# Kernel tuning notes

Hardware: AMD Instinct MI355X
Metric: run time of the kernel (lower is better)

## Reference

```python
import jax, jax.numpy as jnp
import numpy as np

N, E, G = 100000, 3200000, 256
IN_C, HID = 3, 32


def setup_inputs() -> dict:
    key = jax.random.key(0)
    ks = jax.random.split(key, 10)
    x = jax.random.normal(ks[0], (N, IN_C), dtype=jnp.float32)
    edge_index = jax.random.randint(ks[1], (2, E), 0, N, dtype=jnp.int64)
    edge_weight = jax.random.uniform(ks[2], (E,), dtype=jnp.float32)
    batch = jnp.sort(jax.random.randint(ks[3], (N,), 0, G, dtype=jnp.int64))
    # GCNConv params (PyG: out = norm-agg(x @ W) + b), glorot-ish init
    W0 = jax.random.normal(ks[4], (IN_C, HID), dtype=jnp.float32) / np.sqrt(IN_C)
    b0 = jnp.zeros((HID,), dtype=jnp.float32)
    W1 = jax.random.normal(ks[5], (HID, HID), dtype=jnp.float32) / np.sqrt(HID)
    b1 = jnp.zeros((HID,), dtype=jnp.float32)
    Wr = jax.random.normal(ks[6], (HID, 1), dtype=jnp.float32) / np.sqrt(HID)
    br = jnp.zeros((1,), dtype=jnp.float32)
    return {"x": x, "edge_index": edge_index, "edge_weight": edge_weight,
            "batch": batch, "W0": W0, "b0": b0, "W1": W1, "b1": b1,
            "Wr": Wr, "br": br}


def _gcn_conv(x, row, col, w_edge, W, b, n_nodes):
    # PyG GCNConv with add_self_loops + symmetric normalization
    h = x @ W                                   # [N, H]
    deg = jax.ops.segment_sum(w_edge, col, num_segments=n_nodes)
    dinv = jnp.where(deg > 0, jax.lax.rsqrt(deg), 0.0)
    norm = dinv[row] * w_edge * dinv[col]       # [E+N]
    msg = h[row] * norm[:, None]                # gather + scale
    agg = jax.ops.segment_sum(msg, col, num_segments=n_nodes)
    return agg + b


def reference(x, edge_index, edge_weight, batch, W0, b0, W1, b1, Wr, br):
    n = x.shape[0]
    loop = jnp.arange(n, dtype=edge_index.dtype)
    row = jnp.concatenate([edge_index[0], loop])   # source (j)
    col = jnp.concatenate([edge_index[1], loop])   # target (i)
    w = jnp.concatenate([edge_weight, jnp.ones((n,), dtype=edge_weight.dtype)])

    h = jax.nn.relu(_gcn_conv(x, row, col, w, W0, b0, n))
    h = jax.nn.relu(_gcn_conv(h, row, col, w, W1, b1, n))

    # global_mean_pool over graphs
    ones = jnp.ones((n,), dtype=h.dtype)
    cnt = jax.ops.segment_sum(ones, batch, num_segments=G)
    summed = jax.ops.segment_sum(h, batch, num_segments=G)
    hg = summed / jnp.maximum(cnt, 1.0)[:, None]   # [G, H]
    return (hg @ Wr + br).squeeze(-1)              # [G]
```

## Files before the change

### kernel.cpp

```cpp
#include <hip/hip_runtime.h>
#include <hip/hip_fp16.h>


#define TPB 256
#define NBMAX 512
#define BSH 8
#define BSZ 256
#define CAP 9216
#define ST 1024
#define SV 16
#define STILE (ST * SV)

typedef unsigned long long u64;
union H8 { float4 f4; __half2 h2[4]; };
union H4 { u64 u; __half2 h2[2]; };
union HU { __half h; unsigned short u; };

__global__ void k_init(unsigned* cursor, float* gsum, float* gcnt, int nb, int g) {
    int t = threadIdx.x;
    for (int j = t; j < nb; j += blockDim.x) cursor[j] = 0u;
    for (int j = t; j < g; j += blockDim.x) { gsum[j] = 0.0f; gcnt[j] = 0.0f; }
}

__global__ void __launch_bounds__(1024) k_scat(const int* __restrict__ row,
                       const int* __restrict__ col, const float* __restrict__ w,
                       unsigned* cursor, int2* __restrict__ tmp, int nb, int e) {
    __shared__ unsigned cl[NBMAX];
    __shared__ unsigned bl[NBMAX];
    int t = threadIdx.x;
    for (int j = t; j < nb; j += ST) cl[j] = 0u;
    __syncthreads();
    const int4* c4 = (const int4*)col;
    int e4 = e >> 2;
    int base4 = blockIdx.x * (STILE >> 2);
    int4 cv[SV / 4];
    unsigned rk[SV];
    bool vld[SV / 4];
    #pragma unroll
    for (int v = 0; v < SV / 4; ++v) {
        int i4 = base4 + t + v * ST;
        vld[v] = (i4 < e4);
        if (vld[v]) {
            cv[v] = c4[i4];
            rk[4 * v + 0] = atomicAdd(&cl[cv[v].x >> BSH], 1u);
            rk[4 * v + 1] = atomicAdd(&cl[cv[v].y >> BSH], 1u);
            rk[4 * v + 2] = atomicAdd(&cl[cv[v].z >> BSH], 1u);
            rk[4 * v + 3] = atomicAdd(&cl[cv[v].w >> BSH], 1u);
        }
    }
    int tailc = -1; unsigned tailrk = 0; int taili = 0;
    if (blockIdx.x == 0) {
        int i = (e4 << 2) + t;
        if (i < e) { taili = i; tailc = col[i]; tailrk = atomicAdd(&cl[tailc >> BSH], 1u); }
    }
    __syncthreads();
    for (int j = t; j < nb; j += ST) {
        unsigned c = cl[j];
        bl[j] = c ? atomicAdd(&cursor[j], c) : 0u;
    }
    __syncthreads();
    const int4* r4 = (const int4*)row;
    const float4* w4 = (const float4*)w;
    #pragma unroll
    for (int v = 0; v < SV / 4; ++v) {
        if (vld[v]) {
            int i4 = base4 + t + v * ST;
            int4 rr = r4[i4];
            float4 ww = w4[i4];
            int c, b; unsigned lo;
            c = cv[v].x; b = c >> BSH; lo = bl[b] + rk[4 * v + 0];
            if (lo < CAP) tmp[(size_t)b * CAP + lo] =
                make_int2((int)(((unsigned)(c & 255) << 24) | (unsigned)rr.x), __float_as_int(ww.x));
            c = cv[v].y; b = c >> BSH; lo = bl[b] + rk[4 * v + 1];
            if (lo < CAP) tmp[(size_t)b * CAP + lo] =
                make_int2((int)(((unsigned)(c & 255) << 24) | (unsigned)rr.y), __float_as_int(ww.y));
            c = cv[v].z; b = c >> BSH; lo = bl[b] + rk[4 * v + 2];
            if (lo < CAP) tmp[(size_t)b * CAP + lo] =
                make_int2((int)(((unsigned)(c & 255) << 24) | (unsigned)rr.z), __float_as_int(ww.z));
            c = cv[v].w; b = c >> BSH; lo = bl[b] + rk[4 * v + 3];
            if (lo < CAP) tmp[(size_t)b * CAP + lo] =
                make_int2((int)(((unsigned)(c & 255) << 24) | (unsigned)rr.w), __float_as_int(ww.w));
        }
    }
    if (tailc >= 0) {
        int b = tailc >> BSH; unsigned lo = bl[b] + tailrk;
        if (lo < CAP) tmp[(size_t)b * CAP + lo] =
            make_int2((int)(((unsigned)(tailc & 255) << 24) | (unsigned)row[taili]),
                      __float_as_int(w[taili]));
    }
}

__global__ void __launch_bounds__(1024) k_conv(const int2* __restrict__ tmp,
                       const unsigned* __restrict__ cursor, unsigned* __restrict__ nodeinfo,
                       float* __restrict__ dinv, unsigned* __restrict__ arr, int n) {
    __shared__ unsigned cnt[BSZ];
    __shared__ float dw[BSZ];
    __shared__ unsigned cur[BSZ];
    int t = threadIdx.x, b = blockIdx.x;
    if (t < BSZ) { cnt[t] = 0u; dw[t] = 1.0f; }
    __syncthreads();
    unsigned cb = cursor[b]; if (cb > CAP) cb = CAP;
    size_t base = (size_t)b * CAP;
    for (unsigned k = t; k < cb; k += 1024) {
        int2 p = tmp[base + k];
        unsigned c = (unsigned)p.x >> 24;
        atomicAdd(&cnt[c], 1u);
        atomicAdd(&dw[c], __int_as_float(p.y));
    }
    __syncthreads();
    unsigned v = 0;
    if (t < BSZ) { v = cnt[t]; cur[t] = v; }
    __syncthreads();
    for (int off = 1; off < BSZ; off <<= 1) {
        unsigned u = (t < BSZ && t >= off) ? cur[t - off] : 0u;
        __syncthreads();
        if (t < BSZ) cur[t] += u;
        __syncthreads();
    }
    if (t < BSZ) {
        unsigned excl = cur[t] - v;
        int node = (b << BSH) + t;
        if (node < n) {
            unsigned cc = v > 1023u ? 1023u : v;
            nodeinfo[node] = (cc << 22) | (unsigned)(base + excl);
            dinv[node] = rsqrtf(dw[t]);
        }
        cur[t] = excl;
    }
    __syncthreads();
    for (unsigned k = t; k < cb; k += 1024) {
        int2 p = tmp[base + k];
        unsigned c = (unsigned)p.x >> 24;
        unsigned slot = atomicAdd(&cur[c], 1u);
        HU wu; wu.h = __float2half(__int_as_float(p.y));
        arr[base + slot] = ((unsigned)(wu.u & 0x7FFFu) << 17) | ((unsigned)p.x & 0x1FFFFu);
    }
}

__global__ void k_xw0(const float* __restrict__ x, const float* __restrict__ W0,
                      const float* __restrict__ dinv, float4* __restrict__ hw4, int n) {
    int t = blockIdx.x * blockDim.x + threadIdx.x;
    if (t >= n * 4) return;
    int i = t >> 2, q = t & 3;
    float x0 = x[i * 3 + 0], x1 = x[i * 3 + 1], x2 = x[i * 3 + 2];
    float di = dinv[i];
    int cb = q * 8;
    H8 u;
    #pragma unroll
    for (int j = 0; j < 4; ++j) {
        int c = cb + 2 * j;
        float a = di * (x0 * W0[c]     + x1 * W0[32 + c]     + x2 * W0[64 + c]);
        float b = di * (x0 * W0[c + 1] + x1 * W0[32 + c + 1] + x2 * W0[64 + c + 1]);
        u.h2[j] = __float22half2_rn(make_float2(a, b));
    }
    hw4[t] = u.f4;
}

#define EDGE_ACC(V) { \
    unsigned rr = (V) & 0x1FFFFu; \
    HU wu; wu.u = (unsigned short)((V) >> 17); \
    float wv = __half2float(wu.h); \
    H4 g; g.u = hw8[(rr << 3) + q]; \
    float2 f0 = __half22float2(g.h2[0]); \
    float2 f1 = __half22float2(g.h2[1]); \
    a0.x = fmaf(wv, f0.x, a0.x); a0.y = fmaf(wv, f0.y, a0.y); \
    a1.x = fmaf(wv, f1.x, a1.x); a1.y = fmaf(wv, f1.y, a1.y); }

__global__ void __launch_bounds__(256) k_agg1(const u64* __restrict__ hw8,
                      const unsigned* __restrict__ arr, const unsigned* __restrict__ nodeinfo,
                      const float* __restrict__ dinv, const float* __restrict__ W1,
                      const float* __restrict__ b0, u64* __restrict__ out8, int n) {
    __shared__ float W1s[1024];
    __shared__ float hl[32][33];
    int tid = threadIdx.x;
    for (int j = tid; j < 1024; j += 256) W1s[j] = W1[j];
    int t = blockIdx.x * 256 + tid;
    int i = t >> 3, q = t & 7;
    if (i >= n) i = n - 1;
    int li = tid >> 3;
    unsigned info = nodeinfo[i];
    unsigned k = info & 0x3FFFFFu;
    unsigned hi = k + (info >> 22);
    int idx = (i << 3) + q;
    H4 s; s.u = hw8[idx];
    float2 a0 = __half22float2(s.h2[0]);
    float2 a1 = __half22float2(s.h2[1]);
    for (; k + 8 <= hi; k += 8) {
        unsigned v0 = __builtin_nontemporal_load(arr + k + 0);
        unsigned v1 = __builtin_nontemporal_load(arr + k + 1);
        unsigned v2 = __builtin_nontemporal_load(arr + k + 2);
        unsigned v3 = __builtin_nontemporal_load(arr + k + 3);
        unsigned v4 = __builtin_nontemporal_load(arr + k + 4);
        unsigned v5 = __builtin_nontemporal_load(arr + k + 5);
        unsigned v6 = __builtin_nontemporal_load(arr + k + 6);
        unsigned v7 = __builtin_nontemporal_load(arr + k + 7);
        EDGE_ACC(v0) EDGE_ACC(v1) EDGE_ACC(v2) EDGE_ACC(v3)
        EDGE_ACC(v4) EDGE_ACC(v5) EDGE_ACC(v6) EDGE_ACC(v7)
    }
    for (; k < hi; ++k) {
        unsigned v = __builtin_nontemporal_load(arr + k);
        EDGE_ACC(v)
    }
    float di = dinv[i];
    int cb = q << 2;
    hl[li][cb + 0] = fmaxf(di * a0.x + b0[cb + 0], 0.0f);
    hl[li][cb + 1] = fmaxf(di * a0.y + b0[cb + 1], 0.0f);
    hl[li][cb + 2] = fmaxf(di * a1.x + b0[cb + 2], 0.0f);
    hl[li][cb + 3] = fmaxf(di * a1.y + b0[cb + 3], 0.0f);
    __syncthreads();
    float o0 = 0.0f, o1 = 0.0f, o2 = 0.0f, o3 = 0.0f;
    #pragma unroll
    for (int kk = 0; kk < 32; ++kk) {
        float hv = hl[li][kk];
        const float* wr = &W1s[(kk << 5) + cb];
        o0 = fmaf(hv, wr[0], o0);
        o1 = fmaf(hv, wr[1], o1);
        o2 = fmaf(hv, wr[2], o2);
        o3 = fmaf(hv, wr[3], o3);
    }
    H4 oh;
    oh.h2[0] = __float22half2_rn(make_float2(di * o0, di * o1));
    oh.h2[1] = __float22half2_rn(make_float2(di * o2, di * o3));
    out8[idx] = oh.u;
}

__global__ void __launch_bounds__(256) k_agg2(const u64* __restrict__ hw8,
                      const unsigned* __restrict__ arr, const unsigned* __restrict__ nodeinfo,
                      const float* __restrict__ dinv, const float* __restrict__ b1,
                      const float* __restrict__ Wr, const int* __restrict__ batch,
                      float* gsum, float* gcnt, int n) {
    int t = blockIdx.x * 256 + threadIdx.x;
    int i = t >> 3, q = t & 7;
    bool active = (i < n);
    int ii = active ? i : (n - 1);
    unsigned info = active ? nodeinfo[ii] : 0u;
    unsigned k = info & 0x3FFFFFu;
    unsigned hi = k + (info >> 22);
    int idx = (ii << 3) + q;
    H4 s; s.u = hw8[idx];
    float2 a0 = __half22float2(s.h2[0]);
    float2 a1 = __half22float2(s.h2[1]);
    for (; k + 8 <= hi; k += 8) {
        unsigned v0 = __builtin_nontemporal_load(arr + k + 0);
        unsigned v1 = __builtin_nontemporal_load(arr + k + 1);
        unsigned v2 = __builtin_nontemporal_load(arr + k + 2);
        unsigned v3 = __builtin_nontemporal_load(arr + k + 3);
        unsigned v4 = __builtin_nontemporal_load(arr + k + 4);
        unsigned v5 = __builtin_nontemporal_load(arr + k + 5);
        unsigned v6 = __builtin_nontemporal_load(arr + k + 6);
        unsigned v7 = __builtin_nontemporal_load(arr + k + 7);
        EDGE_ACC(v0) EDGE_ACC(v1) EDGE_ACC(v2) EDGE_ACC(v3)
        EDGE_ACC(v4) EDGE_ACC(v5) EDGE_ACC(v6) EDGE_ACC(v7)
    }
    for (; k < hi; ++k) {
        unsigned v = __builtin_nontemporal_load(arr + k);
        EDGE_ACC(v)
    }
    float di = dinv[ii];
    int cb = q << 2;
    float sp = 0.0f;
    sp = fmaf(fmaxf(di * a0.x + b1[cb + 0], 0.0f), Wr[cb + 0], sp);
    sp = fmaf(fmaxf(di * a0.y + b1[cb + 1], 0.0f), Wr[cb + 1], sp);
    sp = fmaf(fmaxf(di * a1.x + b1[cb + 2], 0.0f), Wr[cb + 2], sp);
    sp = fmaf(fmaxf(di * a1.y + b1[cb + 3], 0.0f), Wr[cb + 3], sp);
    if (!active) sp = 0.0f;
    sp += __shfl_xor(sp, 1);
    sp += __shfl_xor(sp, 2);
    sp += __shfl_xor(sp, 4);
    int b = active ? batch[ii] : -1;
    int b0v = __shfl(b, 0, 64);
    bool uniform = (b0v >= 0) && (__ballot(b == b0v) == 0xFFFFFFFFFFFFFFFFULL);
    if (uniform) {
        float tot = sp;
        tot += __shfl_xor(tot, 8);
        tot += __shfl_xor(tot, 16);
        tot += __shfl_xor(tot, 32);
        if ((threadIdx.x & 63) == 0) {
            atomicAdd(&gsum[b0v], tot);
            atomicAdd(&gcnt[b0v], 8.0f);
        }
    } else if (active && q == 0) {
        atomicAdd(&gsum[b], sp);
        atomicAdd(&gcnt[b], 1.0f);
    }
}

__global__ void k_final(const float* gsum, const float* gcnt, const float* __restrict__ br,
                        float* out, int g) {
    int i = blockIdx.x * blockDim.x + threadIdx.x;
    if (i < g) out[i] = gsum[i] / fmaxf(gcnt[i], 1.0f) + br[0];
}

extern "C" void kernel_launch(void* const* d_in, const int* in_sizes, int n_in,
                              void* d_out, int out_size, void* d_ws, size_t ws_size,
                              hipStream_t stream) {
    const float* x     = (const float*)d_in[0];
    const int*   ei    = (const int*)d_in[1];
    const float* ew    = (const float*)d_in[2];
    const int*   batch = (const int*)d_in[3];
    const float* W0    = (const float*)d_in[4];
    const float* b0    = (const float*)d_in[5];
    const float* W1    = (const float*)d_in[6];
    const float* b1    = (const float*)d_in[7];
    const float* Wr    = (const float*)d_in[8];
    const float* br    = (const float*)d_in[9];
    float* out = (float*)d_out;

    int n = in_sizes[0] / 3;
    int e = in_sizes[2];
    int g = out_size;
    const int* row = ei;
    const int* col = ei + e;
    int nb = (n + BSZ - 1) >> BSH;

    char* ws = (char*)d_ws;
    size_t off = 0;
    auto alloc = [&](size_t bytes) -> void* {
        void* p = ws + off;
        off += (bytes + 255) & ~(size_t)255;
        return p;
    };
    unsigned* cursor   = (unsigned*)alloc((size_t)NBMAX * 4);
    unsigned* nodeinfo = (unsigned*)alloc((size_t)n * 4);
    float*    dinv     = (float*)   alloc((size_t)n * 4);
    float*    gsum     = (float*)   alloc((size_t)g * 4);
    float*    gcnt     = (float*)   alloc((size_t)g * 4);
    unsigned* arr      = (unsigned*)alloc((size_t)nb * CAP * 4);
    char*     region   = (char*)    alloc((size_t)nb * CAP * 8);
    int2*   tmp  = (int2*)region;
    __half* hWh1 = (__half*)region;
    __half* hWh2 = (__half*)(region + (size_t)n * 64);
    (void)ws_size;

    int stiles = (e + STILE - 1) / STILE;
    int nq4    = (n * 4 + TPB - 1) / TPB;
    int nq8    = (n * 8 + TPB - 1) / TPB;

    k_init  <<<1,      1024, 0, stream>>>(cursor, gsum, gcnt, nb, g);
    k_scat  <<<stiles, ST,   0, stream>>>(row, col, ew, cursor, tmp, nb, e);
    k_conv  <<<nb,     1024, 0, stream>>>(tmp, cursor, nodeinfo, dinv, arr, n);
    k_xw0   <<<nq4,    TPB,  0, stream>>>(x, W0, dinv, (float4*)hWh1, n);
    k_agg1  <<<nq8,    TPB,  0, stream>>>((const u64*)hWh1, arr, nodeinfo, dinv, W1, b0, (u64*)hWh2, n);
    k_agg2  <<<nq8,    TPB,  0, stream>>>((const u64*)hWh2, arr, nodeinfo, dinv, b1, Wr, batch, gsum, gcnt, n);
    k_final <<<1,      TPB,  0, stream>>>(gsum, gcnt, br, out, g);
}
```

Before: 284.6 us.

## Pack degree count and weight into one 64-bit LDS atomic, split pooling kernel

The scatter kernel's block size drops from 1024 to 512 threads. In the conversion kernel, the per-node edge count and weight sum are packed into one 64-bit shared-memory atomic, with the weight held as 24-bit fixed point, so each edge does one atomic instead of two. The global mean pooling moves out of the second aggregation kernel into a separate kernel that reads one scalar per node, so 64 nodes share a wave's atomics instead of 8. This costs an extra launch and a per-node buffer, and the fixed-point weight sum loses some precision.

```diff
diff --git a/kernel.cpp b/kernel.cpp
--- a/kernel.cpp
+++ b/kernel.cpp
@@ -7,7 +7,7 @@
 #define BSH 8
 #define BSZ 256
 #define CAP 9216
-#define ST 1024
+#define ST 512
 #define SV 16
 #define STILE (ST * SV)
 
@@ -22,7 +22,7 @@
     for (int j = t; j < g; j += blockDim.x) { gsum[j] = 0.0f; gcnt[j] = 0.0f; }
 }
 
-__global__ void __launch_bounds__(1024) k_scat(const int* __restrict__ row,
+__global__ void __launch_bounds__(ST) k_scat(const int* __restrict__ row,
                        const int* __restrict__ col, const float* __restrict__ w,
                        unsigned* cursor, int2* __restrict__ tmp, int nb, int e) {
     __shared__ unsigned cl[NBMAX];
@@ -93,23 +93,29 @@
 __global__ void __launch_bounds__(1024) k_conv(const int2* __restrict__ tmp,
                        const unsigned* __restrict__ cursor, unsigned* __restrict__ nodeinfo,
                        float* __restrict__ dinv, unsigned* __restrict__ arr, int n) {
-    __shared__ unsigned cnt[BSZ];
-    __shared__ float dw[BSZ];
+    __shared__ u64 pk[BSZ];
     __shared__ unsigned cur[BSZ];
     int t = threadIdx.x, b = blockIdx.x;
-    if (t < BSZ) { cnt[t] = 0u; dw[t] = 1.0f; }
+    if (t < BSZ) pk[t] = (u64)(1u << 24);
     __syncthreads();
     unsigned cb = cursor[b]; if (cb > CAP) cb = CAP;
     size_t base = (size_t)b * CAP;
     for (unsigned k = t; k < cb; k += 1024) {
         int2 p = tmp[base + k];
         unsigned c = (unsigned)p.x >> 24;
-        atomicAdd(&cnt[c], 1u);
-        atomicAdd(&dw[c], __int_as_float(p.y));
+        u64 add = (1ull << 48) |
+                  (u64)(unsigned)__float2uint_rn(__int_as_float(p.y) * 16777216.0f);
+        atomicAdd(&pk[c], add);
     }
     __syncthreads();
     unsigned v = 0;
-    if (t < BSZ) { v = cnt[t]; cur[t] = v; }
+    float dwv = 1.0f;
+    if (t < BSZ) {
+        u64 p = pk[t];
+        v = (unsigned)(p >> 48);
+        dwv = (float)(p & 0xFFFFFFFFFFFFull) * (1.0f / 16777216.0f);
+        cur[t] = v;
+    }
     __syncthreads();
     for (int off = 1; off < BSZ; off <<= 1) {
         unsigned u = (t < BSZ && t >= off) ? cur[t - off] : 0u;
@@ -123,7 +129,7 @@
         if (node < n) {
             unsigned cc = v > 1023u ? 1023u : v;
             nodeinfo[node] = (cc << 22) | (unsigned)(base + excl);
-            dinv[node] = rsqrtf(dw[t]);
+            dinv[node] = rsqrtf(dwv);
         }
         cur[t] = excl;
     }
@@ -227,13 +233,12 @@
 __global__ void __launch_bounds__(256) k_agg2(const u64* __restrict__ hw8,
                       const unsigned* __restrict__ arr, const unsigned* __restrict__ nodeinfo,
                       const float* __restrict__ dinv, const float* __restrict__ b1,
-                      const float* __restrict__ Wr, const int* __restrict__ batch,
-                      float* gsum, float* gcnt, int n) {
+                      const float* __restrict__ Wr, float* __restrict__ sout, int n) {
     int t = blockIdx.x * 256 + threadIdx.x;
     int i = t >> 3, q = t & 7;
     bool active = (i < n);
     int ii = active ? i : (n - 1);
-    unsigned info = active ? nodeinfo[ii] : 0u;
+    unsigned info = nodeinfo[ii];
     unsigned k = info & 0x3FFFFFu;
     unsigned hi = k + (info >> 22);
     int idx = (ii << 3) + q;
@@ -263,23 +268,28 @@
     sp = fmaf(fmaxf(di * a0.y + b1[cb + 1], 0.0f), Wr[cb + 1], sp);
     sp = fmaf(fmaxf(di * a1.x + b1[cb + 2], 0.0f), Wr[cb + 2], sp);
     sp = fmaf(fmaxf(di * a1.y + b1[cb + 3], 0.0f), Wr[cb + 3], sp);
-    if (!active) sp = 0.0f;
     sp += __shfl_xor(sp, 1);
     sp += __shfl_xor(sp, 2);
     sp += __shfl_xor(sp, 4);
-    int b = active ? batch[ii] : -1;
+    if (active && q == 0) sout[i] = sp;
+}
+
+__global__ void k_pool2(const float* __restrict__ sarr, const int* __restrict__ batch,
+                        float* gsum, float* gcnt, int n) {
+    int i = blockIdx.x * blockDim.x + threadIdx.x;
+    float sp = 0.0f;
+    int b = -1;
+    if (i < n) { sp = sarr[i]; b = batch[i]; }
     int b0v = __shfl(b, 0, 64);
     bool uniform = (b0v >= 0) && (__ballot(b == b0v) == 0xFFFFFFFFFFFFFFFFULL);
     if (uniform) {
-        float tot = sp;
-        tot += __shfl_xor(tot, 8);
-        tot += __shfl_xor(tot, 16);
-        tot += __shfl_xor(tot, 32);
+        #pragma unroll
+        for (int off = 32; off > 0; off >>= 1) sp += __shfl_down(sp, off, 64);
         if ((threadIdx.x & 63) == 0) {
-            atomicAdd(&gsum[b0v], tot);
-            atomicAdd(&gcnt[b0v], 8.0f);
+            atomicAdd(&gsum[b0v], sp);
+            atomicAdd(&gcnt[b0v], 64.0f);
         }
-    } else if (active && q == 0) {
+    } else if (i < n) {
         atomicAdd(&gsum[b], sp);
         atomicAdd(&gcnt[b], 1.0f);
     }
@@ -323,6 +333,7 @@
     unsigned* cursor   = (unsigned*)alloc((size_t)NBMAX * 4);
     unsigned* nodeinfo = (unsigned*)alloc((size_t)n * 4);
     float*    dinv     = (float*)   alloc((size_t)n * 4);
+    float*    sout     = (float*)   alloc((size_t)n * 4);
     float*    gsum     = (float*)   alloc((size_t)g * 4);
     float*    gcnt     = (float*)   alloc((size_t)g * 4);
     unsigned* arr      = (unsigned*)alloc((size_t)nb * CAP * 4);
@@ -333,6 +344,7 @@
     (void)ws_size;
 
     int stiles = (e + STILE - 1) / STILE;
+    int nbk    = (n + TPB - 1) / TPB;
     int nq4    = (n * 4 + TPB - 1) / TPB;
     int nq8    = (n * 8 + TPB - 1) / TPB;
 
@@ -341,6 +353,7 @@
     k_conv  <<<nb,     1024, 0, stream>>>(tmp, cursor, nodeinfo, dinv, arr, n);
     k_xw0   <<<nq4,    TPB,  0, stream>>>(x, W0, dinv, (float4*)hWh1, n);
     k_agg1  <<<nq8,    TPB,  0, stream>>>((const u64*)hWh1, arr, nodeinfo, dinv, W1, b0, (u64*)hWh2, n);
-    k_agg2  <<<nq8,    TPB,  0, stream>>>((const u64*)hWh2, arr, nodeinfo, dinv, b1, Wr, batch, gsum, gcnt, n);
+    k_agg2  <<<nq8,    TPB,  0, stream>>>((const u64*)hWh2, arr, nodeinfo, dinv, b1, Wr, sout, n);
+    k_pool2 <<<nbk,    TPB,  0, stream>>>(sout, batch, gsum, gcnt, n);
     k_final <<<1,      TPB,  0, stream>>>(gsum, gcnt, br, out, g);
 }
```

Result: no change. 281.0 us (-1.3%).
